# Optimization experiments

Hardware: AMD Instinct MI355X
Metric: run time of the kernel (lower is better)

Reference implementation:

```python
import jax, jax.numpy as jnp
import numpy as np

B, S, D = 2, 2048, 1024
NUM_HEADS = 16
HEAD_DIM = D // NUM_HEADS


def setup_inputs() -> dict:
    key = jax.random.key(0)
    k1, k2, k3, k4 = jax.random.split(key, 4)
    # Weights stored as [d_in, d_out] so projection is x @ W (torch Linear weight transposed).
    scale = 1.0 / np.sqrt(D)
    return {
        "x": jax.random.normal(k1, (B, S, D), dtype=jnp.float32),
        "W_q": jax.random.normal(k2, (D, D), dtype=jnp.float32) * scale,
        "W_k": jax.random.normal(k3, (D, D), dtype=jnp.float32) * scale,
        "W_v": jax.random.normal(k4, (D, D), dtype=jnp.float32) * scale,
    }


def reference(x, W_q, W_k, W_v):
    b, s, d = x.shape
    hd = d // NUM_HEADS
    # QKV projections (no bias, qkv_bias=False)
    q = (x @ W_q).reshape(b, s, NUM_HEADS, hd).transpose(0, 2, 1, 3)  # [B,H,S,hd]
    k = (x @ W_k).reshape(b, s, NUM_HEADS, hd).transpose(0, 2, 1, 3)
    v = (x @ W_v).reshape(b, s, NUM_HEADS, hd).transpose(0, 2, 1, 3)
    # Scaled scores with causal masking (strict upper triangle masked)
    scores = jnp.einsum("bhqd,bhkd->bhqk", q, k) / jnp.sqrt(jnp.float32(hd))
    causal = jnp.triu(jnp.ones((s, s), dtype=bool), 1)  # True = masked
    scores = jnp.where(causal, -jnp.inf, scores)
    attn = jax.nn.softmax(scores, axis=-1)  # dropout is identity (drop_rate=0.0)
    out = jnp.einsum("bhqk,bhkd->bqhd", attn, v).reshape(b, s, d)
    return out
```

## Files before the change

kernel.cpp:

```cpp
#include <hip/hip_runtime.h>


typedef unsigned short u16;
typedef unsigned long long u64;
typedef __bf16 bf16x8 __attribute__((ext_vector_type(8)));
typedef float f32x4 __attribute__((ext_vector_type(4)));
typedef u16 u16x8 __attribute__((ext_vector_type(8)));

#define NB 2
#define NS 2048
#define ND 1024
#define NH 16
#define HD 64

__device__ __forceinline__ u16 f2bf(float f) {
    unsigned int u = __float_as_uint(f);
    unsigned int r = u + 0x7fffu + ((u >> 16) & 1u);
    return (u16)(r >> 16);
}

__device__ __forceinline__ f32x4 mfma16(bf16x8 a, bf16x8 b, f32x4 c) {
    return __builtin_amdgcn_mfma_f32_16x16x32_bf16(a, b, c, 0, 0, 0);
}

__device__ __forceinline__ void gl_lds16(const void* g, void* l) {
    __builtin_amdgcn_global_load_lds(
        (const __attribute__((address_space(1))) unsigned int*)g,
        (__attribute__((address_space(3))) unsigned int*)l, 16, 0, 0);
}

__device__ __forceinline__ bf16x8 ldsw(const u16* base, int row, int colb) {
    return *(const bf16x8*)((const char*)base + row * 128 +
                            (colb ^ ((row & 7) << 4)));
}

__global__ __launch_bounds__(256) void convx_k(const float* __restrict__ x,
                                               u16* __restrict__ xb) {
    int i = (blockIdx.x * 256 + threadIdx.x) * 8;
    const float4* p = (const float4*)(x + i);
    float4 a = p[0], c = p[1];
    u16x8 r;
    r[0] = f2bf(a.x); r[1] = f2bf(a.y); r[2] = f2bf(a.z); r[3] = f2bf(a.w);
    r[4] = f2bf(c.x); r[5] = f2bf(c.y); r[6] = f2bf(c.z); r[7] = f2bf(c.w);
    *(u16x8*)(xb + i) = r;
}

__global__ __launch_bounds__(256) void convw_k(const float* __restrict__ wq,
                                               const float* __restrict__ wk,
                                               const float* __restrict__ wv,
                                               u16* __restrict__ wt) {
    __shared__ float tile[32][33];
    const int z = blockIdx.z;
    const float* W = (z == 0) ? wq : (z == 1) ? wk : wv;
    const int k0 = blockIdx.x * 32, n0 = blockIdx.y * 32;
    const int tx = threadIdx.x & 31, ty = threadIdx.x >> 5;
#pragma unroll
    for (int rr = 0; rr < 32; rr += 8)
        tile[ty + rr][tx] = W[(size_t)(k0 + ty + rr) * ND + n0 + tx];
    __syncthreads();
    u16* dst = wt + (size_t)z * ND * ND;
#pragma unroll
    for (int rr = 0; rr < 32; rr += 8)
        dst[(size_t)(n0 + ty + rr) * ND + k0 + tx] = f2bf(tile[tx][ty + rr]);
}

__global__ __launch_bounds__(256) void qkv_gemm_k(const u16* __restrict__ xb,
                                                  const u16* __restrict__ wt,
                                                  u16* __restrict__ qh,
                                                  u16* __restrict__ kh,
                                                  u16* __restrict__ vt) {
    __shared__ u16 At[128 * 64];
    __shared__ u16 Bt[3][64 * 64];
    const int m0 = blockIdx.x * 128;
    const int n0 = blockIdx.y * 64;
    const int t = threadIdx.x;
    const int lane = t & 63;
    const int wv = t >> 6;
    const int wm = (wv >> 1) * 64, wn = (wv & 1) * 32;
    const int fr = lane & 15;
    const int ks = lane >> 4;

    f32x4 acc[3][4][2] = {};

    for (int kt = 0; kt < ND; kt += 64) {
#pragma unroll
        for (int c = 0; c < 4; c++) {
            const int L = c * 4096 + t * 16;
            const int row = L >> 7;
            const int cb = (L & 127) ^ ((row & 7) << 4);
            gl_lds16((const char*)xb + (size_t)(m0 + row) * 2048 + kt * 2 + cb,
                     (char*)At + L);
        }
#pragma unroll
        for (int z = 0; z < 3; z++)
#pragma unroll
            for (int c = 0; c < 2; c++) {
                const int L = c * 4096 + t * 16;
                const int row = L >> 7;
                const int cb = (L & 127) ^ ((row & 7) << 4);
                gl_lds16((const char*)wt + (size_t)z * (ND * ND * 2) +
                             (size_t)(n0 + row) * 2048 + kt * 2 + cb,
                         (char*)&Bt[z][0] + L);
            }
        __syncthreads();

        bf16x8 fa[4][2];
#pragma unroll
        for (int i = 0; i < 4; i++)
#pragma unroll
            for (int c = 0; c < 2; c++)
                fa[i][c] = ldsw(At, wm + i * 16 + fr, c * 64 + ks * 16);

#pragma unroll
        for (int z = 0; z < 3; z++) {
            bf16x8 fb[2][2];
#pragma unroll
            for (int j = 0; j < 2; j++)
#pragma unroll
                for (int c = 0; c < 2; c++)
                    fb[j][c] =
                        ldsw(&Bt[z][0], wn + j * 16 + fr, c * 64 + ks * 16);
            if (z < 2) {
#pragma unroll
                for (int i = 0; i < 4; i++)
#pragma unroll
                    for (int j = 0; j < 2; j++)
#pragma unroll
                        for (int c = 0; c < 2; c++)
                            acc[z][i][j] =
                                mfma16(fa[i][c], fb[j][c], acc[z][i][j]);
            } else {
#pragma unroll
                for (int i = 0; i < 4; i++)
#pragma unroll
                    for (int j = 0; j < 2; j++)
#pragma unroll
                        for (int c = 0; c < 2; c++)
                            acc[z][i][j] =
                                mfma16(fb[j][c], fa[i][c], acc[z][i][j]);
            }
        }
        __syncthreads();
    }

#pragma unroll
    for (int z = 0; z < 2; z++) {
        u16* dst = (z == 0) ? qh : kh;
#pragma unroll
        for (int i = 0; i < 4; i++)
#pragma unroll
            for (int j = 0; j < 2; j++)
#pragma unroll
                for (int r = 0; r < 4; r++) {
                    int mg = m0 + wm + i * 16 + ks * 4 + r;
                    int ng = n0 + wn + j * 16 + fr;
                    int b = mg >> 11, s = mg & 2047;
                    int hh = ng >> 6, dd = ng & 63;
                    dst[(((size_t)b * NH + hh) * NS + s) * HD + dd] =
                        f2bf(acc[z][i][j][r]);
                }
    }
#pragma unroll
    for (int i = 0; i < 4; i++)
#pragma unroll
        for (int j = 0; j < 2; j++)
#pragma unroll
            for (int r = 0; r < 4; r++) {
                int ng = n0 + wn + j * 16 + ks * 4 + r;
                int mg = m0 + wm + i * 16 + fr;
                int b = mg >> 11, s = mg & 2047;
                int hh = ng >> 6, dd = ng & 63;
                int w = s & 63;
                int sp = (s & ~63) | (w & 32) | (((w >> 2) & 3) << 3) |
                         (((w >> 4) & 1) << 2) | (w & 3);
                vt[(((size_t)b * NH + hh) * HD + dd) * NS + sp] =
                    f2bf(acc[2][i][j][r]);
            }
}


__device__ __forceinline__ void stage_kv(const u16* __restrict__ K,
                                         const u16* __restrict__ V, int kv0,
                                         u16* Kl, u16* Vl, int t) {
#pragma unroll
    for (int c = 0; c < 2; c++) {
        const int L = c * 4096 + t * 16;
        const int row = L >> 7;
        const int cb = (L & 127) ^ ((row & 7) << 4);
        gl_lds16((const char*)K + (size_t)(kv0 + row) * 128 + cb,
                 (char*)Kl + L);
        gl_lds16((const char*)V + (size_t)row * (NS * 2) + kv0 * 2 + cb,
                 (char*)Vl + L);
    }
}

template <bool MASKED>
__device__ __forceinline__ void sm_pack(const f32x4* sc, bf16x8 pa[2],
                                        int kv0, int q0, int fr, int ks) {
    const int qg = q0 + fr;
#pragma unroll
    for (int kf = 0; kf < 4; kf++)
#pragma unroll
        for (int r = 0; r < 4; r++) {
            float s = sc[kf][r];
            if (MASKED && (kv0 + kf * 16 + ks * 4 + r > qg)) s = -3.0e38f;
            pa[kf >> 1][(kf & 1) * 4 + r] =
                (__bf16)exp2f(fmaf(s, 0.18033688f, -11.5415603f));
        }
}

__device__ __forceinline__ void pv_reg(const bf16x8 (*fv)[2],
                                       const bf16x8 pa[2], f32x4* o,
                                       f32x4& lacc, bf16x8 ones) {
    __builtin_amdgcn_s_setprio(1);
    lacc = mfma16(pa[0], ones, lacc);
    lacc = mfma16(pa[1], ones, lacc);
#pragma unroll
    for (int j = 0; j < 4; j++)
#pragma unroll
        for (int s2 = 0; s2 < 2; s2++) o[j] = mfma16(pa[s2], fv[j][s2], o[j]);
    __builtin_amdgcn_s_setprio(0);
}

__global__ __launch_bounds__(256) void attn_k(const u16* __restrict__ qh,
                                              const u16* __restrict__ kh,
                                              const u16* __restrict__ vt,
                                              float* __restrict__ out) {
    const int t = threadIdx.x, lane = t & 63, wv = t >> 6;
    const int fr = lane & 15, ks = lane >> 4;
    const int bh = blockIdx.x & 31;
    const int tile = 31 - (int)(blockIdx.x >> 5);
    const int b = bh >> 4, h = bh & 15;
    const int q0 = tile * 64 + wv * 16;
    const int nIt = tile + 1;
    const u16* Q = qh + (size_t)bh * NS * HD;
    const u16* K = kh + (size_t)bh * NS * HD;
    const u16* V = vt + (size_t)bh * HD * NS;

    __shared__ u16 Kl[2][64 * 64];
    __shared__ u16 Vl[2][64 * 64];

    bf16x8 fq[2];
#pragma unroll
    for (int sl = 0; sl < 2; sl++)
        fq[sl] = *(const bf16x8*)&Q[(q0 + fr) * HD + sl * 32 + ks * 8];

    u16x8 ob;
#pragma unroll
    for (int j = 0; j < 8; j++) ob[j] = 0x3F80;
    const bf16x8 ones = __builtin_bit_cast(bf16x8, ob);

    f32x4 o[4] = {};
    f32x4 l = {};

    stage_kv(K, V, 0, &Kl[0][0], &Vl[0][0], t);
    __syncthreads();

    for (int it = 0; it < nIt; ++it) {
        const int cur = it & 1;
        const int kv0 = it * 64;
        if (it + 1 < nIt)
            stage_kv(K, V, kv0 + 64, &Kl[cur ^ 1][0], &Vl[cur ^ 1][0], t);

        bf16x8 fk[4][2];
#pragma unroll
        for (int kf = 0; kf < 4; kf++)
#pragma unroll
            for (int sl = 0; sl < 2; sl++)
                fk[kf][sl] =
                    ldsw(&Kl[cur][0], kf * 16 + fr, sl * 64 + ks * 16);

        f32x4 sc[4] = {};
        __builtin_amdgcn_s_setprio(1);
#pragma unroll
        for (int kf = 0; kf < 4; kf++) {
            sc[kf] = mfma16(fk[kf][0], fq[0], sc[kf]);
            sc[kf] = mfma16(fk[kf][1], fq[1], sc[kf]);
        }
        __builtin_amdgcn_s_setprio(0);

        bf16x8 fv[4][2];
#pragma unroll
        for (int j = 0; j < 4; j++)
#pragma unroll
            for (int s2 = 0; s2 < 2; s2++)
                fv[j][s2] =
                    ldsw(&Vl[cur][0], j * 16 + fr, s2 * 64 + ks * 16);

        bf16x8 pa[2];
        if (it == nIt - 1)
            sm_pack<true>(sc, pa, kv0, q0, fr, ks);
        else
            sm_pack<false>(sc, pa, kv0, q0, fr, ks);
        pv_reg(fv, pa, o, l, ones);

        __syncthreads();
    }

    float rl[4];
#pragma unroll
    for (int r = 0; r < 4; r++) rl[r] = 1.0f / l[r];
#pragma unroll
    for (int j = 0; j < 4; j++)
#pragma unroll
        for (int r = 0; r < 4; r++) {
            const int qg = q0 + ks * 4 + r;
            out[((size_t)b * NS + qg) * ND + h * HD + j * 16 + fr] =
                o[j][r] * rl[r];
        }
}

extern "C" void kernel_launch(void* const* d_in, const int* in_sizes, int n_in,
                              void* d_out, int out_size, void* d_ws,
                              size_t ws_size, hipStream_t stream) {
    const float* x = (const float*)d_in[0];
    const float* wq = (const float*)d_in[1];
    const float* wk = (const float*)d_in[2];
    const float* wvp = (const float*)d_in[3];
    float* out = (float*)d_out;

    char* w8 = (char*)d_ws;
    u16* xb = (u16*)(w8);
    u16* wt = (u16*)(w8 + ((size_t)8 << 20));
    u16* qh = (u16*)(w8 + ((size_t)14 << 20));
    u16* kh = (u16*)(w8 + ((size_t)22 << 20));
    u16* vt = (u16*)(w8 + ((size_t)30 << 20));

    convx_k<<<(NB * NS * ND) / (256 * 8), 256, 0, stream>>>(x, xb);
    convw_k<<<dim3(ND / 32, ND / 32, 3), 256, 0, stream>>>(wq, wk, wvp, wt);
    qkv_gemm_k<<<dim3((NB * NS) / 128, ND / 64), 256, 0, stream>>>(
        xb, wt, qh, kh, vt);
    attn_k<<<1024, 256, 0, stream>>>(qh, kh, vt, out);
}
```

Baseline: 82.59 us.

## Split long causal attention tiles across two blocks and combine partials

The upper half of the query tiles (tiles 16-31) now have their KV range split between two blocks. Each block writes an unnormalized partial output in bf16 plus its row-sum to workspace, and a new combine kernel adds the partials and normalizes. This is meant to fix the load imbalance from causal masking, where the last tiles do up to 32 iterations, by giving more, shorter blocks (1536 instead of 1024). The cost is an extra kernel launch, extra global traffic, and bf16 rounding of the partial outputs. The combine relies on the softmax having no running max subtraction, so the partials add directly.

New measurement: 87.94 us. +6.5%, slower.

```diff
diff --git a/kernel.cpp b/kernel.cpp
--- a/kernel.cpp
+++ b/kernel.cpp
@@ -2,6 +2,7 @@
 
 
 typedef unsigned short u16;
+typedef unsigned int u32;
 typedef unsigned long long u64;
 typedef __bf16 bf16x8 __attribute__((ext_vector_type(8)));
 typedef float f32x4 __attribute__((ext_vector_type(4)));
@@ -225,14 +226,31 @@
 __global__ __launch_bounds__(256) void attn_k(const u16* __restrict__ qh,
                                               const u16* __restrict__ kh,
                                               const u16* __restrict__ vt,
-                                              float* __restrict__ out) {
+                                              float* __restrict__ out,
+                                              u16* __restrict__ opart,
+                                              float* __restrict__ lpart) {
     const int t = threadIdx.x, lane = t & 63, wv = t >> 6;
     const int fr = lane & 15, ks = lane >> 4;
     const int bh = blockIdx.x & 31;
-    const int tile = 31 - (int)(blockIdx.x >> 5);
+    const int u = blockIdx.x >> 5;
     const int b = bh >> 4, h = bh & 15;
+    int tile, half, s0, s1;
+    bool split;
+    if (u < 32) {
+        tile = 31 - (u >> 1);
+        half = u & 1;
+        const int n = tile + 1, n0 = (n + 1) >> 1;
+        s0 = half ? n0 : 0;
+        s1 = half ? n : n0;
+        split = true;
+    } else {
+        tile = 47 - u;
+        half = 0;
+        s0 = 0;
+        s1 = tile + 1;
+        split = false;
+    }
     const int q0 = tile * 64 + wv * 16;
-    const int nIt = tile + 1;
     const u16* Q = qh + (size_t)bh * NS * HD;
     const u16* K = kh + (size_t)bh * NS * HD;
     const u16* V = vt + (size_t)bh * HD * NS;
@@ -253,13 +271,13 @@
     f32x4 o[4] = {};
     f32x4 l = {};
 
-    stage_kv(K, V, 0, &Kl[0][0], &Vl[0][0], t);
+    stage_kv(K, V, s0 * 64, &Kl[0][0], &Vl[0][0], t);
     __syncthreads();
 
-    for (int it = 0; it < nIt; ++it) {
-        const int cur = it & 1;
+    for (int it = s0; it < s1; ++it) {
+        const int cur = (it - s0) & 1;
         const int kv0 = it * 64;
-        if (it + 1 < nIt)
+        if (it + 1 < s1)
             stage_kv(K, V, kv0 + 64, &Kl[cur ^ 1][0], &Vl[cur ^ 1][0], t);
 
         bf16x8 fk[4][2];
@@ -288,7 +306,7 @@
                     ldsw(&Vl[cur][0], j * 16 + fr, s2 * 64 + ks * 16);
 
         bf16x8 pa[2];
-        if (it == nIt - 1)
+        if (it == tile)
             sm_pack<true>(sc, pa, kv0, q0, fr, ks);
         else
             sm_pack<false>(sc, pa, kv0, q0, fr, ks);
@@ -297,17 +315,70 @@
         __syncthreads();
     }
 
-    float rl[4];
-#pragma unroll
-    for (int r = 0; r < 4; r++) rl[r] = 1.0f / l[r];
-#pragma unroll
-    for (int j = 0; j < 4; j++)
-#pragma unroll
-        for (int r = 0; r < 4; r++) {
-            const int qg = q0 + ks * 4 + r;
-            out[((size_t)b * NS + qg) * ND + h * HD + j * 16 + fr] =
-                o[j][r] * rl[r];
+    if (!split) {
+        float rl[4];
+#pragma unroll
+        for (int r = 0; r < 4; r++) rl[r] = 1.0f / l[r];
+#pragma unroll
+        for (int j = 0; j < 4; j++)
+#pragma unroll
+            for (int r = 0; r < 4; r++) {
+                const int qg = q0 + ks * 4 + r;
+                out[((size_t)b * NS + qg) * ND + h * HD + j * 16 + fr] =
+                    o[j][r] * rl[r];
+            }
+    } else {
+        const int base = (half * 32 + bh) * 1024;
+#pragma unroll
+        for (int j = 0; j < 4; j++)
+#pragma unroll
+            for (int r = 0; r < 4; r++) {
+                const int sp = q0 - 1024 + ks * 4 + r;
+                opart[((size_t)(base + sp) << 6) + j * 16 + fr] =
+                    f2bf(o[j][r]);
+            }
+        if (fr == 0) {
+#pragma unroll
+            for (int r = 0; r < 4; r++)
+                lpart[base + q0 - 1024 + ks * 4 + r] = l[r];
         }
+    }
+}
+
+__global__ __launch_bounds__(256) void comb_k(const u16* __restrict__ opart,
+                                              const float* __restrict__ lpart,
+                                              float* __restrict__ out) {
+    const int idx = blockIdx.x * 256 + threadIdx.x;
+    const int e = idx * 8;
+    const int d0 = e & 63;
+    const int row = e >> 6;
+    const int sp = row & 1023, bh = row >> 10;
+    const int b = bh >> 4, h = bh & 15;
+    const u16x8 o0 = *(const u16x8*)&opart[((size_t)(bh * 1024 + sp) << 6) + d0];
+    const u16x8 o1 =
+        *(const u16x8*)&opart[((size_t)((32 + bh) * 1024 + sp) << 6) + d0];
+    const float rl =
+        1.0f / (lpart[bh * 1024 + sp] + lpart[32768 + bh * 1024 + sp]);
+    float* dst = &out[((size_t)b * NS + 1024 + sp) * ND + h * HD + d0];
+    float4 w0, w1;
+    w0.x = (__uint_as_float((u32)o0[0] << 16) +
+            __uint_as_float((u32)o1[0] << 16)) * rl;
+    w0.y = (__uint_as_float((u32)o0[1] << 16) +
+            __uint_as_float((u32)o1[1] << 16)) * rl;
+    w0.z = (__uint_as_float((u32)o0[2] << 16) +
+            __uint_as_float((u32)o1[2] << 16)) * rl;
+    w0.w = (__uint_as_float((u32)o0[3] << 16) +
+            __uint_as_float((u32)o1[3] << 16)) * rl;
+    w1.x = (__uint_as_float((u32)o0[4] << 16) +
+            __uint_as_float((u32)o1[4] << 16)) * rl;
+    w1.y = (__uint_as_float((u32)o0[5] << 16) +
+            __uint_as_float((u32)o1[5] << 16)) * rl;
+    w1.z = (__uint_as_float((u32)o0[6] << 16) +
+            __uint_as_float((u32)o1[6] << 16)) * rl;
+    w1.w = (__uint_as_float((u32)o0[7] << 16) +
+            __uint_as_float((u32)o1[7] << 16)) * rl;
+    *(float4*)dst = w0;
+    *(float4*)(dst + 4) = w1;
 }
 
 extern "C" void kernel_launch(void* const* d_in, const int* in_sizes, int n_in,
@@ -325,10 +396,13 @@
     u16* qh = (u16*)(w8 + ((size_t)14 << 20));
     u16* kh = (u16*)(w8 + ((size_t)22 << 20));
     u16* vt = (u16*)(w8 + ((size_t)30 << 20));
+    u16* opart = (u16*)(w8);
+    float* lpart = (float*)(w8 + ((size_t)9 << 20));
 
     convx_k<<<(NB * NS * ND) / (256 * 8), 256, 0, stream>>>(x, xb);
     convw_k<<<dim3(ND / 32, ND / 32, 3), 256, 0, stream>>>(wq, wk, wvp, wt);
     qkv_gemm_k<<<dim3((NB * NS) / 128, ND / 64), 256, 0, stream>>>(
         xb, wt, qh, kh, vt);
-    attn_k<<<1024, 256, 0, stream>>>(qh, kh, vt, out);
-}
+    attn_k<<<1536, 256, 0, stream>>>(qh, kh, vt, out, opart, lpart);
+    comb_k<<<1024, 256, 0, stream>>>(opart, lpart, out);
+}
```
